# Kernel tuning notes

Hardware: AMD Instinct MI355X
Metric: run time of the kernel (lower is better)

## Reference

```python
import jax, jax.numpy as jnp
import numpy as np

ROPE_BASE = 10000.0

def apply_rope(x):
    # x: (BS, T, H, hd). 1D RoPE over temporal axis with rotate-half convention.
    BS, T, H, hd = x.shape
    half = hd // 2
    inv_freq = 1.0 / (ROPE_BASE ** (jnp.arange(0, half, dtype=jnp.float32) / half))
    angles = jnp.arange(T, dtype=jnp.float32)[:, None] * inv_freq[None, :]  # (T, half)
    cos = jnp.concatenate([jnp.cos(angles), jnp.cos(angles)], axis=-1)[None, :, None, :]  # (1,T,1,hd)
    sin = jnp.concatenate([jnp.sin(angles), jnp.sin(angles)], axis=-1)[None, :, None, :]
    x1, x2 = x[..., :half], x[..., half:]
    x_rot = jnp.concatenate([-x2, x1], axis=-1)
    return (x * cos + x_rot * sin).astype(x.dtype)

def setup_inputs() -> dict:
    key = jax.random.key(0)
    ks = jax.random.split(key, 7)
    B, T_p, T_f, S, d = 4, 8, 8, 256, 512
    v_p = jax.random.normal(ks[0], (B, T_p, S, d), dtype=jnp.float32)
    v_f = jax.random.normal(ks[1], (B, T_f, S, d), dtype=jnp.float32)
    a_p = jax.random.normal(ks[2], (B, T_p, d), dtype=jnp.float32)
    a_f = jax.random.normal(ks[3], (B, T_f, d), dtype=jnp.float32)
    W_qkv = jax.random.normal(ks[4], (d, 3 * d), dtype=jnp.float32) * (d ** -0.5)
    W_proj = jax.random.normal(ks[5], (d, d), dtype=jnp.float32) * (d ** -0.5)
    b_proj = jnp.zeros((d,), dtype=jnp.float32)
    return {"v_p": v_p, "v_f": v_f, "a_p": a_p, "a_f": a_f,
            "W_qkv": W_qkv, "W_proj": W_proj, "b_proj": b_proj}

def reference(v_p, v_f, a_p, a_f, W_qkv, W_proj, b_proj):
    num_heads = 8
    B, T_p, S, d = v_p.shape
    T_f = v_f.shape[1]
    hd = d // num_heads
    scale = hd ** -0.5

    # rearrange 'b t s d -> (b s) t d'
    vp = jnp.transpose(v_p, (0, 2, 1, 3)).reshape(B * S, T_p, d)
    vf = jnp.transpose(v_f, (0, 2, 1, 3)).reshape(B * S, T_f, d)
    # repeat 'b t d -> (b s) t d'
    ap = jnp.broadcast_to(a_p[:, None], (B, S, T_p, d)).reshape(B * S, T_p, d)
    af = jnp.broadcast_to(a_f[:, None], (B, S, T_f, d)).reshape(B * S, T_f, d)

    tokens = jnp.concatenate([vp, vf, ap, af], axis=1)  # (BS, total_T, d)
    BS, total_T = tokens.shape[0], tokens.shape[1]

    qkv = tokens @ W_qkv  # (BS, total_T, 3d), no bias
    q, k, v = jnp.split(qkv, 3, axis=-1)
    q = q.reshape(BS, total_T, num_heads, hd)
    k = k.reshape(BS, total_T, num_heads, hd)
    v = v.reshape(BS, total_T, num_heads, hd)

    q = apply_rope(q)
    k = apply_rope(k)

    # joint bidirectional attention over total_T
    attn = jnp.einsum('bthd,bThd->bhtT', q, k) * scale
    attn = jax.nn.softmax(attn, axis=-1)
    out = jnp.einsum('bhtT,bThd->bthd', attn, v).reshape(BS, total_T, d)

    out = out @ W_proj + b_proj

    vp_o = out[:, :T_p]
    vf_o = out[:, T_p:T_p + T_f]
    ap_o = out[:, T_p + T_f:T_p + T_f + T_p]
    af_o = out[:, T_p + T_f + T_p:]

    # '(b s) t d -> b t s d'
    vp_o = jnp.transpose(vp_o.reshape(B, S, T_p, d), (0, 2, 1, 3))
    vf_o = jnp.transpose(vf_o.reshape(B, S, T_f, d), (0, 2, 1, 3))
    # '(b s) t d -> b s t d' then mean over s
    ap_o = ap_o.reshape(B, S, T_p, d).mean(axis=1)
    af_o = af_o.reshape(B, S, T_f, d).mean(axis=1)
    return (vp_o, vf_o, ap_o, af_o)
```

## Files before the change

kernel.cpp:

```cpp
#include <hip/hip_runtime.h>
#include <math.h>

#define BB   4
#define SS   256
#define DD   512
#define HH   8
#define HD   64
#define HALF 32
#define TT   32
#define TV   16
#define W3   1536
#define MROWS  16448
#define MPAD   16512

#define VP_BASE 0
#define VF_BASE 4194304
#define AP_BASE 8388608
#define AF_BASE 8404992

#define LN10000_OVER_HALF (9.210340371976184f / 32.0f)

typedef _Float16 h2 __attribute__((ext_vector_type(2)));
typedef _Float16 h4 __attribute__((ext_vector_type(4)));
typedef _Float16 h8 __attribute__((ext_vector_type(8)));
typedef float    f4 __attribute__((ext_vector_type(4)));
typedef float    f16v __attribute__((ext_vector_type(16)));

__device__ __forceinline__ float ropefreq(int i) {
    return __expf(-(float)i * LN10000_OVER_HALF);
}

typedef __attribute__((address_space(3))) void*       lds_ptr_t;
typedef const __attribute__((address_space(1))) void* gbl_ptr_t;
__device__ __forceinline__ void async16(const void* g, void* l) {
    __builtin_amdgcn_global_load_lds((gbl_ptr_t)g, (lds_ptr_t)l, 16, 0, 0);
}

__device__ __forceinline__ int xcd_swz(int bid, int nwg) {
    int q = nwg >> 3, r = nwg & 7;
    int xcd = bid & 7, off = bid >> 3;
    return (xcd < r ? xcd * (q + 1) : r * (q + 1) + (xcd - r) * q) + off;
}

__global__ __launch_bounds__(256)
void conv_kernel(const float* __restrict__ v_p, const float* __restrict__ v_f,
                 const float* __restrict__ a_p, const float* __restrict__ a_f,
                 const float* __restrict__ Wqkv, const float* __restrict__ Wp,
                 _Float16* __restrict__ tok, _Float16* __restrict__ Wt,
                 _Float16* __restrict__ Wpt, float2* __restrict__ rope) {
    __shared__ float tile[64 * 65];
    const int bid = blockIdx.x, tid = threadIdx.x;
    if (bid < 8224) {
        int id = bid * 256 + tid;
        int e  = id * 4;
        int r  = e >> 9, c = e & 511;
        const float* src;
        if (r < 16384) {
            int bs = r >> 4, t = r & 15, b = bs >> 8, s = bs & 255;
            src = (t < 8) ? v_p + (size_t)((b * 8 + t) * SS + s) * DD
                          : v_f + (size_t)((b * 8 + t - 8) * SS + s) * DD;
        } else {
            int idx = r - 16384, b = idx >> 4, t2 = idx & 15;
            src = (t2 < 8) ? a_p + (size_t)(b * 8 + t2) * DD
                           : a_f + (size_t)(b * 8 + (t2 - 8)) * DD;
        }
        float4 v = *(const float4*)(src + c);
        h4 o = { (_Float16)v.x, (_Float16)v.y, (_Float16)v.z, (_Float16)v.w };
        *(h4*)(tok + (size_t)r * DD + c) = o;
    } else if (bid < 8480) {
        int tb = bid - 8224;
        const float* src; _Float16* dst; int ld, k0, n0;
        if (tb < 192) {
            src = Wqkv; dst = Wt; ld = W3;
            k0 = (tb & 7) * 64; n0 = (tb >> 3) * 64;
        } else {
            int t2 = tb - 192;
            src = Wp; dst = Wpt; ld = DD;
            k0 = (t2 & 7) * 64; n0 = (t2 >> 3) * 64;
        }
#pragma unroll
        for (int p = 0; p < 16; ++p) {
            int idx = p * 256 + tid, rr = idx >> 6, cc = idx & 63;
            tile[rr * 65 + cc] = src[(size_t)(k0 + rr) * ld + n0 + cc];
        }
        __syncthreads();
#pragma unroll
        for (int p = 0; p < 16; ++p) {
            int idx = p * 256 + tid, rr = idx >> 6, cc = idx & 63;
            dst[(size_t)(n0 + rr) * DD + k0 + cc] = (_Float16)tile[cc * 65 + rr];
        }
    } else {
        int idx = tid * 4;
#pragma unroll
        for (int e2 = 0; e2 < 4; ++e2) {
            int ii = (idx + e2) & 31, tt = (idx + e2) >> 5;
            float ang = (float)tt * ropefreq(ii);
            float sn, cs;
            __sincosf(ang, &sn, &cs);
            rope[idx + e2] = make_float2(cs, sn);
        }
    }
}

__global__ __launch_bounds__(256, 3)
void gemm_qkv_kernel(const _Float16* __restrict__ A, const _Float16* __restrict__ Bt,
                     _Float16* __restrict__ C) {
    __shared__ __align__(16) _Float16 As[128 * 64];
    __shared__ __align__(16) _Float16 Bs[128 * 64];
    const int tid = threadIdx.x, lane = tid & 63, wave = tid >> 6;
    const int bid = xcd_swz(blockIdx.x, 129 * 12);
    const int tm = bid / 12, tn = bid % 12;
    const int m_base = (wave >> 1) * 64, n_base = (wave & 1) * 64;
    const int quad = lane >> 4, l16 = lane & 15;

    f4 acc[4][4] = {};

    int srow[4], soff[4];
#pragma unroll
    for (int p = 0; p < 4; ++p) {
        int ci = p * 256 + tid;
        int r = ci >> 3, sl = ci & 7;
        srow[p] = r;
        soff[p] = (sl ^ (r & 7)) * 8;
    }

    for (int k0 = 0; k0 < 512; k0 += 64) {
#pragma unroll
        for (int p = 0; p < 4; ++p) {
            int ci = p * 256 + tid;
            async16(A  + (size_t)(tm * 128 + srow[p]) * 512 + k0 + soff[p],
                    &As[ci * 8]);
            async16(Bt + (size_t)(tn * 128 + srow[p]) * 512 + k0 + soff[p],
                    &Bs[ci * 8]);
        }
        __syncthreads();

#pragma unroll
        for (int kk = 0; kk < 2; ++kk) {
            h8 af[4], bf[4];
#pragma unroll
            for (int mi = 0; mi < 4; ++mi) {
                int m = m_base + mi * 16 + l16;
                int sl = (kk * 4 + quad) ^ (m & 7);
                af[mi] = *(const h8*)&As[m * 64 + sl * 8];
            }
#pragma unroll
            for (int ni = 0; ni < 4; ++ni) {
                int n = n_base + ni * 16 + l16;
                int sl = (kk * 4 + quad) ^ (n & 7);
                bf[ni] = *(const h8*)&Bs[n * 64 + sl * 8];
            }
#pragma unroll
            for (int mi = 0; mi < 4; ++mi)
#pragma unroll
                for (int ni = 0; ni < 4; ++ni)
                    acc[mi][ni] = __builtin_amdgcn_mfma_f32_16x16x32_f16(
                        af[mi], bf[ni], acc[mi][ni], 0, 0, 0);
        }
        __syncthreads();
    }

#pragma unroll
    for (int mi = 0; mi < 4; ++mi)
#pragma unroll
        for (int ni = 0; ni < 4; ++ni) {
            int row = tm * 128 + m_base + mi * 16 + quad * 4;
            int col = tn * 128 + n_base + ni * 16 + l16;
#pragma unroll
            for (int r = 0; r < 4; ++r)
                C[(size_t)(row + r) * W3 + col] = (_Float16)acc[mi][ni][r];
        }
}

__global__ __launch_bounds__(256)
void attn5_kernel(const _Float16* __restrict__ qkv, const float2* __restrict__ rope,
                  _Float16* __restrict__ attnv, _Float16* __restrict__ attna) {
    __shared__ _Float16 VlA[4][32 * 72];
    __shared__ _Float16 PlA[4][32 * 40];
    const int bid = blockIdx.x;
    const int bs = bid >> 1, hh = bid & 1, b = bs >> 8, s = bs & 255;
    const int tid = threadIdx.x, wave = tid >> 6, lane = tid & 63;
    const int t = lane & 31, half = lane >> 5;
    _Float16* vl = &VlA[wave][0];
    _Float16* pl = &PlA[wave][0];
    const int h = wave + 4 * hh;

    const size_t row = (t < 16) ? (size_t)(bs * 16 + t)
                                : (size_t)(16384 + b * 16 + (t - 16));
    const _Float16* qp = qkv + row * W3 + h * HD;

    float ccA[8], ssA[8], ccB[8], ssB[8];
    const float2* rt = rope + t * 32 + 8 * half;
#pragma unroll
    for (int j = 0; j < 8; ++j) {
        float2 eA = rt[j];
        float2 eB = rt[16 + j];
        ccA[j] = eA.x; ssA[j] = eA.y;
        ccB[j] = eB.x; ssB[j] = eB.y;
    }

    h8 v0 = *(const h8*)(qp + 2 * DD + 32 * half);
    h8 v1 = *(const h8*)(qp + 2 * DD + 32 * half + 8);
    h8 v2 = *(const h8*)(qp + 2 * DD + 32 * half + 16);
    h8 v3 = *(const h8*)(qp + 2 * DD + 32 * half + 24);
    *(h8*)&vl[t * 72 + 32 * half +  0] = v0;
    *(h8*)&vl[t * 72 + 32 * half +  8] = v1;
    *(h8*)&vl[t * 72 + 32 * half + 16] = v2;
    *(h8*)&vl[t * 72 + 32 * half + 24] = v3;

    h8 q0 = *(const h8*)(qp + 8 * half);
    h8 q1 = *(const h8*)(qp + 8 * half + 16);
    h8 q2 = *(const h8*)(qp + 8 * half + 32);
    h8 q3 = *(const h8*)(qp + 8 * half + 48);
    h8 k0 = *(const h8*)(qp + DD + 8 * half);
    h8 k1 = *(const h8*)(qp + DD + 8 * half + 16);
    h8 k2 = *(const h8*)(qp + DD + 8 * half + 32);
    h8 k3 = *(const h8*)(qp + DD + 8 * half + 48);

    h8 qf0, qf1, qf2, qf3, kf0, kf1, kf2, kf3;
#pragma unroll
    for (int j = 0; j < 8; ++j) {
        float x1 = (float)q0[j], x2 = (float)q2[j];
        qf0[j] = (_Float16)(0.125f * (x1 * ccA[j] - x2 * ssA[j]));
        qf2[j] = (_Float16)(0.125f * (x2 * ccA[j] + x1 * ssA[j]));
        x1 = (float)q1[j]; x2 = (float)q3[j];
        qf1[j] = (_Float16)(0.125f * (x1 * ccB[j] - x2 * ssB[j]));
        qf3[j] = (_Float16)(0.125f * (x2 * ccB[j] + x1 * ssB[j]));
        x1 = (float)k0[j]; x2 = (float)k2[j];
        kf0[j] = (_Float16)(x1 * ccA[j] - x2 * ssA[j]);
        kf2[j] = (_Float16)(x2 * ccA[j] + x1 * ssA[j]);
        x1 = (float)k1[j]; x2 = (float)k3[j];
        kf1[j] = (_Float16)(x1 * ccB[j] - x2 * ssB[j]);
        kf3[j] = (_Float16)(x2 * ccB[j] + x1 * ssB[j]);
    }

    f16v s4 = {};
    s4 = __builtin_amdgcn_mfma_f32_32x32x16_f16(qf0, kf0, s4, 0, 0, 0);
    s4 = __builtin_amdgcn_mfma_f32_32x32x16_f16(qf1, kf1, s4, 0, 0, 0);
    s4 = __builtin_amdgcn_mfma_f32_32x32x16_f16(qf2, kf2, s4, 0, 0, 0);
    s4 = __builtin_amdgcn_mfma_f32_32x32x16_f16(qf3, kf3, s4, 0, 0, 0);

#pragma unroll
    for (int r = 0; r < 16; ++r) {
        float e = __expf(s4[r]);
        int rr = (r & 3) + 8 * (r >> 2) + 4 * half;
        pl[rr * 40 + t] = (_Float16)e;
    }

    h8 onesv;
#pragma unroll
    for (int j = 0; j < 8; ++j) onesv[j] = (_Float16)1.0f;

    h8 pf[2];
#pragma unroll
    for (int kk = 0; kk < 2; ++kk)
        pf[kk] = *(const h8*)&pl[t * 40 + kk * 16 + half * 8];

    f16v o1 = {};
#pragma unroll
    for (int kk = 0; kk < 2; ++kk)
        o1 = __builtin_amdgcn_mfma_f32_32x32x16_f16(pf[kk], onesv, o1, 0, 0, 0);

    f16v o_acc[2];
#pragma unroll
    for (int n0 = 0; n0 < 2; ++n0) {
        f16v o = {};
#pragma unroll
        for (int kk = 0; kk < 2; ++kk) {
            h8 vf;
#pragma unroll
            for (int jj = 0; jj < 8; ++jj)
                vf[jj] = vl[(kk * 16 + half * 8 + jj) * 72 + n0 * 32 + t];
            o = __builtin_amdgcn_mfma_f32_32x32x16_f16(pf[kk], vf, o, 0, 0, 0);
        }
        o_acc[n0] = o;
    }

#pragma unroll
    for (int r = 0; r < 16; ++r) {
        float inv = __builtin_amdgcn_rcpf(o1[r]);
        o_acc[0][r] *= inv;
        o_acc[1][r] *= inv;
    }

#pragma unroll
    for (int n0 = 0; n0 < 2; ++n0)
#pragma unroll
        for (int r = 0; r < 16; ++r) {
            int i = (r & 3) + 8 * (r >> 2) + 4 * half;
            vl[i * 72 + n0 * 32 + t] = (_Float16)o_acc[n0][r];
        }

#pragma unroll
    for (int rr = 0; rr < 4; ++rr) {
        int i = rr * 8 + (lane >> 3);
        int c = (lane & 7) * 8;
        h8 val = *(const h8*)&vl[i * 72 + c];
        if (rr < 2)
            *(h8*)&attnv[(size_t)(bs * 16 + i) * DD + h * HD + c] = val;
        else
            *(h8*)&attna[(((size_t)b * 16 + (i - 16)) * SS + s) * DD + h * HD + c] = val;
    }
}

__global__ __launch_bounds__(256)
void reduce_a_kernel(const _Float16* __restrict__ attna, _Float16* __restrict__ abar) {
    __shared__ float red[16][128];
    const int bid = blockIdx.x;
    const int r = bid >> 2, cq = bid & 3;
    const int tid = threadIdx.x;
    const int rg = tid >> 4, ch = tid & 15;

    float acc[8] = {};
    const _Float16* base = attna + ((size_t)r * SS + rg * 16) * DD + cq * 128 + ch * 8;
#pragma unroll 4
    for (int i = 0; i < 16; ++i) {
        h8 v = *(const h8*)(base + (size_t)i * DD);
#pragma unroll
        for (int j = 0; j < 8; ++j) acc[j] += (float)v[j];
    }
#pragma unroll
    for (int j = 0; j < 8; ++j) red[rg][ch * 8 + j] = acc[j];
    __syncthreads();

    if (tid < 64) {
        int c = tid * 2;
        float s0 = 0.f, s1 = 0.f;
#pragma unroll
        for (int g = 0; g < 16; ++g) { s0 += red[g][c]; s1 += red[g][c + 1]; }
        h2 o = { (_Float16)(s0 * (1.0f / SS)), (_Float16)(s1 * (1.0f / SS)) };
        *(h2*)&abar[(size_t)r * DD + cq * 128 + c] = o;
    }
}

__global__ __launch_bounds__(256, 3)
void proj_kernel(const _Float16* __restrict__ A, const _Float16* __restrict__ Bt,
                 const float* __restrict__ bp, float* __restrict__ out) {
    __shared__ __align__(16) _Float16 As[128 * 64];
    __shared__ __align__(16) _Float16 Bs[128 * 64];
    const int tid = threadIdx.x, lane = tid & 63, wave = tid >> 6;
    const int bid = xcd_swz(blockIdx.x, 129 * 4);
    const int tm = bid >> 2, tn = bid & 3;
    const int m_base = (wave >> 1) * 64, n_base = (wave & 1) * 64;
    const int quad = lane >> 4, l16 = lane & 15;

    f4 acc[4][4] = {};

    int srow[4], soff[4];
#pragma unroll
    for (int p = 0; p < 4; ++p) {
        int ci = p * 256 + tid;
        int r = ci >> 3, sl = ci & 7;
        srow[p] = r;
        soff[p] = (sl ^ (r & 7)) * 8;
    }

    for (int k0 = 0; k0 < 512; k0 += 64) {
#pragma unroll
        for (int p = 0; p < 4; ++p) {
            int ci = p * 256 + tid;
            async16(A  + (size_t)(tm * 128 + srow[p]) * 512 + k0 + soff[p],
                    &As[ci * 8]);
            async16(Bt + (size_t)(tn * 128 + srow[p]) * 512 + k0 + soff[p],
                    &Bs[ci * 8]);
        }
        __syncthreads();

#pragma unroll
        for (int kk = 0; kk < 2; ++kk) {
            h8 af[4], bf[4];
#pragma unroll
            for (int mi = 0; mi < 4; ++mi) {
                int m = m_base + mi * 16 + l16;
                int sl = (kk * 4 + quad) ^ (m & 7);
                af[mi] = *(const h8*)&As[m * 64 + sl * 8];
            }
#pragma unroll
            for (int ni = 0; ni < 4; ++ni) {
                int n = n_base + ni * 16 + l16;
                int sl = (kk * 4 + quad) ^ (n & 7);
                bf[ni] = *(const h8*)&Bs[n * 64 + sl * 8];
            }
#pragma unroll
            for (int mi = 0; mi < 4; ++mi)
#pragma unroll
                for (int ni = 0; ni < 4; ++ni)
                    acc[mi][ni] = __builtin_amdgcn_mfma_f32_16x16x32_f16(
                        af[mi], bf[ni], acc[mi][ni], 0, 0, 0);
        }
        __syncthreads();
    }

#pragma unroll
    for (int mi = 0; mi < 4; ++mi)
#pragma unroll
        for (int ni = 0; ni < 4; ++ni) {
            int row0 = tm * 128 + m_base + mi * 16 + quad * 4;
            int col  = tn * 128 + n_base + ni * 16 + l16;
            float bias = bp[col];
#pragma unroll
            for (int r = 0; r < 4; ++r) {
                int row = row0 + r;
                float val = acc[mi][ni][r] + bias;
                if (row < 16384) {
                    int bsq = row >> 4, t = row & 15;
                    int b = bsq >> 8, s = bsq & 255;
                    size_t off = (t < 8)
                        ? (VP_BASE + (size_t)((b * 8 + t) * SS + s) * DD + col)
                        : (VF_BASE + (size_t)((b * 8 + t - 8) * SS + s) * DD + col);
                    out[off] = val;
                } else if (row < 16448) {
                    int idx = row - 16384;
                    int b = idx >> 4, t2 = idx & 15;
                    size_t off = (t2 < 8)
                        ? (AP_BASE + (size_t)(b * 8 + t2) * DD + col)
                        : (AF_BASE + (size_t)(b * 8 + (t2 - 8)) * DD + col);
                    out[off] = val;
                }
            }
        }
}

extern "C" void kernel_launch(void* const* d_in, const int* in_sizes, int n_in,
                              void* d_out, int out_size, void* d_ws, size_t ws_size,
                              hipStream_t stream) {
    const float* v_p  = (const float*)d_in[0];
    const float* v_f  = (const float*)d_in[1];
    const float* a_p  = (const float*)d_in[2];
    const float* a_f  = (const float*)d_in[3];
    const float* Wqkv = (const float*)d_in[4];
    const float* Wp   = (const float*)d_in[5];
    const float* bp   = (const float*)d_in[6];
    float* out = (float*)d_out;

    char* w = (char*)d_ws;
    _Float16* tok   = (_Float16*)w;  w += (size_t)MPAD * DD * 2;
    _Float16* qkv   = (_Float16*)w;  w += (size_t)MPAD * W3 * 2;
    _Float16* attnv = (_Float16*)w;  w += (size_t)MPAD * DD * 2;
    _Float16* Wt    = (_Float16*)w;  w += (size_t)W3 * DD * 2;
    _Float16* Wpt   = (_Float16*)w;  w += (size_t)DD * DD * 2;
    float2*   rope  = (float2*)w;    w += (size_t)1024 * sizeof(float2);
    _Float16* attna = tok;
    _Float16* abar  = attnv + (size_t)16384 * DD;

    conv_kernel<<<8481, 256, 0, stream>>>(v_p, v_f, a_p, a_f, Wqkv, Wp,
                                          tok, Wt, Wpt, rope);
    gemm_qkv_kernel<<<129 * 12, 256, 0, stream>>>(tok, Wt, qkv);
    attn5_kernel<<<2048, 256, 0, stream>>>(qkv, rope, attnv, attna);
    reduce_a_kernel<<<256, 256, 0, stream>>>(attna, abar);
    proj_kernel<<<129 * 4, 256, 0, stream>>>(attnv, Wpt, bp, out);
}
```

Measured before the change: 174.5 us.

## Fuse audio-token mean reduction into attention via float atomics

Removes the separate reduce kernel and the 32 MB fp16 staging buffer for per-(b,s) audio attention outputs. Each attention block now atomically adds its audio-token outputs into a small fp32 accumulator, which conv_kernel zeroes in an extra block. The projection kernel's last M-tile reads that accumulator, scales it by 1/S and converts it to fp16 in LDS. The cost is heavy atomic contention: 256 s-blocks add into the same 128x512 addresses, and summation order becomes nondeterministic.

Result: slower. 407.3 us (+133.3%).

```diff
diff --git a/kernel.cpp b/kernel.cpp
--- a/kernel.cpp
+++ b/kernel.cpp
@@ -47,7 +47,8 @@
                  const float* __restrict__ a_p, const float* __restrict__ a_f,
                  const float* __restrict__ Wqkv, const float* __restrict__ Wp,
                  _Float16* __restrict__ tok, _Float16* __restrict__ Wt,
-                 _Float16* __restrict__ Wpt, float2* __restrict__ rope) {
+                 _Float16* __restrict__ Wpt, float2* __restrict__ rope,
+                 float* __restrict__ aaccum) {
     __shared__ float tile[64 * 65];
     const int bid = blockIdx.x, tid = threadIdx.x;
     if (bid < 8224) {
@@ -89,7 +90,7 @@
             int idx = p * 256 + tid, rr = idx >> 6, cc = idx & 63;
             dst[(size_t)(n0 + rr) * DD + k0 + cc] = (_Float16)tile[cc * 65 + rr];
         }
-    } else {
+    } else if (bid == 8480) {
         int idx = tid * 4;
 #pragma unroll
         for (int e2 = 0; e2 < 4; ++e2) {
@@ -99,6 +100,11 @@
             __sincosf(ang, &sn, &cs);
             rope[idx + e2] = make_float2(cs, sn);
         }
+    } else {
+        f4 z = {};
+#pragma unroll
+        for (int p = 0; p < 64; ++p)
+            *(f4*)&aaccum[(p * 256 + tid) * 4] = z;
     }
 }
 
@@ -174,7 +180,7 @@
 
 __global__ __launch_bounds__(256)
 void attn5_kernel(const _Float16* __restrict__ qkv, const float2* __restrict__ rope,
-                  _Float16* __restrict__ attnv, _Float16* __restrict__ attna) {
+                  _Float16* __restrict__ attnv, float* __restrict__ aaccum) {
     __shared__ _Float16 VlA[4][32 * 72];
     __shared__ _Float16 PlA[4][32 * 40];
     const int bid = blockIdx.x;
@@ -296,46 +302,21 @@
         int i = rr * 8 + (lane >> 3);
         int c = (lane & 7) * 8;
         h8 val = *(const h8*)&vl[i * 72 + c];
-        if (rr < 2)
+        if (rr < 2) {
             *(h8*)&attnv[(size_t)(bs * 16 + i) * DD + h * HD + c] = val;
-        else
-            *(h8*)&attna[(((size_t)b * 16 + (i - 16)) * SS + s) * DD + h * HD + c] = val;
-    }
-}
-
-__global__ __launch_bounds__(256)
-void reduce_a_kernel(const _Float16* __restrict__ attna, _Float16* __restrict__ abar) {
-    __shared__ float red[16][128];
-    const int bid = blockIdx.x;
-    const int r = bid >> 2, cq = bid & 3;
-    const int tid = threadIdx.x;
-    const int rg = tid >> 4, ch = tid & 15;
-
-    float acc[8] = {};
-    const _Float16* base = attna + ((size_t)r * SS + rg * 16) * DD + cq * 128 + ch * 8;
-#pragma unroll 4
-    for (int i = 0; i < 16; ++i) {
-        h8 v = *(const h8*)(base + (size_t)i * DD);
-#pragma unroll
-        for (int j = 0; j < 8; ++j) acc[j] += (float)v[j];
-    }
-#pragma unroll
-    for (int j = 0; j < 8; ++j) red[rg][ch * 8 + j] = acc[j];
-    __syncthreads();
-
-    if (tid < 64) {
-        int c = tid * 2;
-        float s0 = 0.f, s1 = 0.f;
-#pragma unroll
-        for (int g = 0; g < 16; ++g) { s0 += red[g][c]; s1 += red[g][c + 1]; }
-        h2 o = { (_Float16)(s0 * (1.0f / SS)), (_Float16)(s1 * (1.0f / SS)) };
-        *(h2*)&abar[(size_t)r * DD + cq * 128 + c] = o;
+        } else {
+            float* dst = aaccum + (size_t)(b * 16 + (i - 16)) * DD + h * HD + c;
+#pragma unroll
+            for (int j = 0; j < 8; ++j)
+                atomicAdd(dst + j, (float)val[j]);
+        }
     }
 }
 
 __global__ __launch_bounds__(256, 3)
-void proj_kernel(const _Float16* __restrict__ A, const _Float16* __restrict__ Bt,
-                 const float* __restrict__ bp, float* __restrict__ out) {
+void proj_kernel(const _Float16* __restrict__ A, const float* __restrict__ aaccum,
+                 const _Float16* __restrict__ Bt, const float* __restrict__ bp,
+                 float* __restrict__ out) {
     __shared__ __align__(16) _Float16 As[128 * 64];
     __shared__ __align__(16) _Float16 Bs[128 * 64];
     const int tid = threadIdx.x, lane = tid & 63, wave = tid >> 6;
@@ -343,6 +324,7 @@
     const int tm = bid >> 2, tn = bid & 3;
     const int m_base = (wave >> 1) * 64, n_base = (wave & 1) * 64;
     const int quad = lane >> 4, l16 = lane & 15;
+    const float INV = 1.0f / (float)SS;
 
     f4 acc[4][4] = {};
 
@@ -356,11 +338,30 @@
     }
 
     for (int k0 = 0; k0 < 512; k0 += 64) {
+        if (tm < 128) {
+#pragma unroll
+            for (int p = 0; p < 4; ++p) {
+                int ci = p * 256 + tid;
+                async16(A + (size_t)(tm * 128 + srow[p]) * 512 + k0 + soff[p],
+                        &As[ci * 8]);
+            }
+        } else {
+#pragma unroll
+            for (int p = 0; p < 4; ++p) {
+                int ci = p * 256 + tid;
+                const float* sp = aaccum + (size_t)srow[p] * 512 + k0 + soff[p];
+                float4 w0 = *(const float4*)(sp);
+                float4 w1 = *(const float4*)(sp + 4);
+                h8 o = { (_Float16)(w0.x * INV), (_Float16)(w0.y * INV),
+                         (_Float16)(w0.z * INV), (_Float16)(w0.w * INV),
+                         (_Float16)(w1.x * INV), (_Float16)(w1.y * INV),
+                         (_Float16)(w1.z * INV), (_Float16)(w1.w * INV) };
+                *(h8*)&As[ci * 8] = o;
+            }
+        }
 #pragma unroll
         for (int p = 0; p < 4; ++p) {
             int ci = p * 256 + tid;
-            async16(A  + (size_t)(tm * 128 + srow[p]) * 512 + k0 + soff[p],
-                    &As[ci * 8]);
             async16(Bt + (size_t)(tn * 128 + srow[p]) * 512 + k0 + soff[p],
                     &Bs[ci * 8]);
         }
@@ -440,13 +441,11 @@
     _Float16* Wt    = (_Float16*)w;  w += (size_t)W3 * DD * 2;
     _Float16* Wpt   = (_Float16*)w;  w += (size_t)DD * DD * 2;
     float2*   rope  = (float2*)w;    w += (size_t)1024 * sizeof(float2);
-    _Float16* attna = tok;
-    _Float16* abar  = attnv + (size_t)16384 * DD;
-
-    conv_kernel<<<8481, 256, 0, stream>>>(v_p, v_f, a_p, a_f, Wqkv, Wp,
-                                          tok, Wt, Wpt, rope);
+    float*    aaccum= (float*)w;     w += (size_t)128 * DD * sizeof(float);
+
+    conv_kernel<<<8482, 256, 0, stream>>>(v_p, v_f, a_p, a_f, Wqkv, Wp,
+                                          tok, Wt, Wpt, rope, aaccum);
     gemm_qkv_kernel<<<129 * 12, 256, 0, stream>>>(tok, Wt, qkv);
-    attn5_kernel<<<2048, 256, 0, stream>>>(qkv, rope, attnv, attna);
-    reduce_a_kernel<<<256, 256, 0, stream>>>(attna, abar);
-    proj_kernel<<<129 * 4, 256, 0, stream>>>(attnv, Wpt, bp, out);
-}
+    attn5_kernel<<<2048, 256, 0, stream>>>(qkv, rope, attnv, aaccum);
+    proj_kernel<<<129 * 4, 256, 0, stream>>>(attnv, aaccum, Wpt, bp, out);
+}
```
